# Optimization experiments

Hardware: AMD Instinct MI355X
Metric: run time of the kernel (lower is better)

Reference implementation:

```python
import jax, jax.numpy as jnp
import numpy as np

EMBED = 256; DEPTH = 64; DEPTH_START = 1.0
POS_RANGE = (-61.2, -61.2, -10.0, 61.2, 61.2, 10.0)
PC_RANGE = (-51.2, -51.2, -5.0, 51.2, 51.2, 3.0)
MEM_LEN = 512; TOPK = 256; NUM_Q = 900; NUM_CLS = 10; CODE = 10; L = 6
B, N, H, W = 4, 6, 16, 44
PAD_H, PAD_W = 256, 704
TWO_PI = 2.0 * np.pi


def _posemb(coords, nf=128):
    # sine/cosine embedding per coordinate channel -> [..., C, nf]
    dim_t = 10000.0 ** (2.0 * (jnp.arange(nf, dtype=jnp.float32) // 2) / nf)
    p = (coords * TWO_PI)[..., None] / dim_t
    p = jnp.stack([jnp.sin(p[..., 0::2]), jnp.cos(p[..., 1::2])], -1)
    return p.reshape(p.shape[:-2] + (nf,))


def _mlp2(x, W1, b1, W2, b2):
    return jnp.maximum(x @ W1 + b1, 0.0) @ W2 + b2


def _conv1x1(x, Wt, b):
    return jnp.einsum('bchw,co->bohw', x, Wt) + b[None, :, None, None]


def _ln(x, g, b):
    m = jnp.mean(x, -1, keepdims=True)
    v = jnp.mean(jnp.square(x - m), -1, keepdims=True)
    return (x - m) / jnp.sqrt(v + 1e-5) * g + b


def _sine_pe(not_mask):
    # SinePositionalEncoding2D, normalize=True; not_mask: [BN,H,W] float
    nf = EMBED // 2; eps = 1e-6
    y = jnp.cumsum(not_mask, 1); x = jnp.cumsum(not_mask, 2)
    y = y / (y[:, -1:, :] + eps) * TWO_PI
    x = x / (x[:, :, -1:] + eps) * TWO_PI
    dim_t = 10000.0 ** (2.0 * (jnp.arange(nf, dtype=jnp.float32) // 2) / nf)
    px = x[..., None] / dim_t; py = y[..., None] / dim_t
    px = jnp.stack([jnp.sin(px[..., 0::2]), jnp.cos(px[..., 1::2])], -1).reshape(x.shape + (nf,))
    py = jnp.stack([jnp.sin(py[..., 0::2]), jnp.cos(py[..., 1::2])], -1).reshape(y.shape + (nf,))
    return jnp.concatenate([py, px], -1).transpose(0, 3, 1, 2)  # [BN,EMBED,H,W]


def _forward(feat, lidar2img, prev_exists, memory_embedding, memory_reference_point,
             memory_timestamp, outs_dec, ref_pts, ip_w, ip_b, pe_w1, pe_b1, pe_w2, pe_b2,
             ap_w1, ap_b1, ap_w2, ap_b2, qe_w1, qe_b1, qe_w2, qe_b2, te_w1, te_b1, te_w2,
             te_b2, cls_w1, cls_b1, cls_g1, cls_be1, cls_w2, cls_b2, cls_g2, cls_be2,
             cls_w3, cls_b3, reg_w1, reg_b1, reg_w2, reg_b2, reg_w3, reg_b3, masks):
    b, n, c, h, w = feat.shape
    # --- pre_update_memory: memory_refresh + timestamp advance ---
    prev = prev_exists.reshape(b, 1, 1)
    mem_e = memory_embedding * prev
    mem_r = memory_reference_point * prev
    mem_t = memory_timestamp * prev + prev
    # --- input projection (1x1 conv) ---
    x = _conv1x1(feat.reshape(b * n, c, h, w), ip_w, ip_b).reshape(b, n, EMBED, h, w)
    # --- 3D position embedding (PETR frustum) ---
    coords_h = jnp.arange(h, dtype=jnp.float32) * (float(PAD_H) / h)
    coords_w = jnp.arange(w, dtype=jnp.float32) * (float(PAD_W) / w)
    d = jnp.arange(DEPTH, dtype=jnp.float32)
    bin_size = (POS_RANGE[3] - DEPTH_START) / (DEPTH * (1.0 + DEPTH))
    coords_d = DEPTH_START + bin_size * d * (d + 1.0)  # LID discretization
    cw, ch_, cd = jnp.meshgrid(coords_w, coords_h, coords_d, indexing='ij')  # [W,H,D]
    xy = jnp.stack([cw, ch_], -1) * jnp.maximum(cd, 1e-5)[..., None]
    coords4 = jnp.concatenate([xy, cd[..., None], jnp.ones_like(cd[..., None])], -1)  # [W,H,D,4]
    img2lidars = jnp.linalg.inv(lidar2img)  # [B,N,4,4]
    c3 = jnp.einsum('bnij,whdj->bnwhdi', img2lidars, coords4)[..., :3]  # [B,N,W,H,D,3]
    lo = jnp.asarray(POS_RANGE[:3], jnp.float32); hi = jnp.asarray(POS_RANGE[3:], jnp.float32)
    c3 = (c3 - lo) / (hi - lo)
    cmask = ((c3 > 1.0) | (c3 < 0.0)).reshape(b, n, w, h, DEPTH * 3).sum(-1) > DEPTH * 0.5
    coords_mask = masks | cmask.transpose(0, 1, 3, 2)
    c3 = c3.transpose(0, 1, 4, 5, 3, 2).reshape(b * n, DEPTH * 3, h, w)
    c3 = jnp.clip(c3, 0.0, 1.0)
    c3 = jnp.log(jnp.clip(c3, 1e-5, None) / jnp.clip(1.0 - c3, 1e-5, None))  # inverse_sigmoid
    coords_pos = _conv1x1(jnp.maximum(_conv1x1(c3, pe_w1, pe_b1), 0.0), pe_w2, pe_b2)
    coords_pos = coords_pos.reshape(b, n, EMBED, h, w)
    # --- 2D sine PE + adapt_pos3d ---
    sine = _sine_pe((~masks).astype(jnp.float32).reshape(b * n, h, w))
    sine = _conv1x1(jnp.maximum(_conv1x1(sine, ap_w1, ap_b1), 0.0), ap_w2, ap_b2)
    pos_embed = coords_pos + sine.reshape(b, n, EMBED, h, w)
    # --- query / time embeddings ---
    qp = _posemb(ref_pts)  # [Q,3,128]
    qp = jnp.concatenate([qp[:, 1], qp[:, 0], qp[:, 2]], -1)  # (y,x,z) -> [Q,384]
    query_pos = _mlp2(qp, qe_w1, qe_b1, qe_w2, qe_b2)  # [Q,256]
    tp = _posemb(mem_t)[..., 0, :]  # [B,M,128]
    time_emb = _mlp2(tp, te_w1, te_b1, te_w2, te_b2)  # [B,M,256]
    # --- cls / reg branches, stacked over decoder layers ---
    hc = jnp.maximum(_ln(jnp.einsum('lbqd,lde->lbqe', outs_dec, cls_w1) + cls_b1[:, None, None], cls_g1[:, None, None], cls_be1[:, None, None]), 0.0)
    hc = jnp.maximum(_ln(jnp.einsum('lbqd,lde->lbqe', hc, cls_w2) + cls_b2[:, None, None], cls_g2[:, None, None], cls_be2[:, None, None]), 0.0)
    all_cls = jnp.einsum('lbqd,ldc->lbqc', hc, cls_w3) + cls_b3[:, None, None]
    hr = jnp.maximum(jnp.einsum('lbqd,lde->lbqe', outs_dec, reg_w1) + reg_b1[:, None, None], 0.0)
    hr = jnp.maximum(jnp.einsum('lbqd,lde->lbqe', hr, reg_w2) + reg_b2[:, None, None], 0.0)
    all_reg = jnp.einsum('lbqd,ldc->lbqc', hr, reg_w3) + reg_b3[:, None, None]
    # --- post_update_memory: sigmoid + topk + gather + rolling concat ---
    rec_score = jnp.max(jax.nn.sigmoid(all_cls[-1]), -1)  # topk(1) over classes == max
    _, idx = jax.lax.top_k(rec_score, TOPK)  # [B,K]
    rec_mem = jax.lax.stop_gradient(jnp.take_along_axis(outs_dec[-1], idx[..., None], axis=1))
    rec_ref = jax.lax.stop_gradient(jnp.take_along_axis(all_reg[-1][..., :3], idx[..., None], axis=1))
    pmin = jnp.asarray(PC_RANGE[:3], jnp.float32); pmax = jnp.asarray(PC_RANGE[3:], jnp.float32)
    rec_ref = jnp.clip((rec_ref - pmin) / jnp.clip(pmax - pmin, 1e-5, None), 0.0, 1.0)
    rec_ts = jnp.zeros((b, TOPK, 1), rec_mem.dtype)
    new_mem_e = jnp.concatenate([rec_mem, mem_e], 1)[:, :MEM_LEN]
    new_mem_r = jnp.concatenate([rec_ref, mem_r], 1)[:, :MEM_LEN]
    new_mem_t = jnp.concatenate([rec_ts, mem_t], 1)[:, :MEM_LEN]
    return (all_cls, all_reg, new_mem_e, new_mem_r, new_mem_t, pos_embed, x, query_pos, time_emb, coords_mask)


def setup_inputs() -> dict:
    key = jax.random.key(0)
    ks = jax.random.split(key, 24)
    def rn(k, shape, s=0.02):
        return jax.random.normal(k, shape, jnp.float32) * s
    inp = dict(
        feat=jax.random.normal(ks[0], (B, N, 256, H, W), jnp.float32),
        lidar2img=jnp.eye(4, dtype=jnp.float32) + 0.05 * jax.random.normal(ks[1], (B, N, 4, 4), jnp.float32),
        prev_exists=jnp.array([1.0, 0.0, 1.0, 1.0], jnp.float32),
        memory_embedding=jax.random.normal(ks[2], (B, MEM_LEN, EMBED), jnp.float32),
        memory_reference_point=jax.random.uniform(ks[3], (B, MEM_LEN, 3)),
        memory_timestamp=jax.random.uniform(ks[4], (B, MEM_LEN, 1)),
        outs_dec=jax.random.normal(ks[5], (L, B, NUM_Q, EMBED), jnp.float32),
        ref_pts=jax.random.uniform(ks[6], (NUM_Q, 3)),
        ip_w=rn(ks[7], (256, EMBED)), ip_b=jnp.zeros(EMBED),
        pe_w1=rn(ks[8], (3 * DEPTH, EMBED * 2)), pe_b1=jnp.zeros(EMBED * 2),
        pe_w2=rn(ks[9], (EMBED * 2, EMBED)), pe_b2=jnp.zeros(EMBED),
        ap_w1=rn(ks[10], (EMBED, EMBED)), ap_b1=jnp.zeros(EMBED),
        ap_w2=rn(ks[11], (EMBED, EMBED)), ap_b2=jnp.zeros(EMBED),
        qe_w1=rn(ks[12], (EMBED * 3 // 2, EMBED)), qe_b1=jnp.zeros(EMBED),
        qe_w2=rn(ks[13], (EMBED, EMBED)), qe_b2=jnp.zeros(EMBED),
        te_w1=rn(ks[14], (EMBED // 2, EMBED)), te_b1=jnp.zeros(EMBED),
        te_w2=rn(ks[15], (EMBED, EMBED)), te_b2=jnp.zeros(EMBED),
        cls_w1=rn(ks[16], (L, EMBED, EMBED)), cls_b1=jnp.zeros((L, EMBED)),
        cls_g1=jnp.ones((L, EMBED)), cls_be1=jnp.zeros((L, EMBED)),
        cls_w2=rn(ks[17], (L, EMBED, EMBED)), cls_b2=jnp.zeros((L, EMBED)),
        cls_g2=jnp.ones((L, EMBED)), cls_be2=jnp.zeros((L, EMBED)),
        cls_w3=rn(ks[18], (L, EMBED, NUM_CLS)), cls_b3=jnp.zeros((L, NUM_CLS)),
        reg_w1=rn(ks[19], (L, EMBED, EMBED)), reg_b1=jnp.zeros((L, EMBED)),
        reg_w2=rn(ks[20], (L, EMBED, EMBED)), reg_b2=jnp.zeros((L, EMBED)),
        reg_w3=rn(ks[21], (L, EMBED, CODE)), reg_b3=jnp.zeros((L, CODE)),
        masks=jnp.zeros((B, N, H, W), bool),
    )
    return inp


def reference(feat, lidar2img, prev_exists, memory_embedding, memory_reference_point,
              memory_timestamp, outs_dec, ref_pts, ip_w, ip_b, pe_w1, pe_b1, pe_w2, pe_b2,
              ap_w1, ap_b1, ap_w2, ap_b2, qe_w1, qe_b1, qe_w2, qe_b2, te_w1, te_b1, te_w2,
              te_b2, cls_w1, cls_b1, cls_g1, cls_be1, cls_w2, cls_b2, cls_g2, cls_be2,
              cls_w3, cls_b3, reg_w1, reg_b1, reg_w2, reg_b2, reg_w3, reg_b3, masks):
    return _forward(feat, lidar2img, prev_exists, memory_embedding, memory_reference_point,
                    memory_timestamp, outs_dec, ref_pts, ip_w, ip_b, pe_w1, pe_b1, pe_w2, pe_b2,
                    ap_w1, ap_b1, ap_w2, ap_b2, qe_w1, qe_b1, qe_w2, qe_b2, te_w1, te_b1, te_w2,
                    te_b2, cls_w1, cls_b1, cls_g1, cls_be1, cls_w2, cls_b2, cls_g2, cls_be2,
                    cls_w3, cls_b3, reg_w1, reg_b1, reg_w2, reg_b2, reg_w3, reg_b3, masks)
```

## Files before the change

### kernel.cpp

```cpp
#include <hip/hip_runtime.h>
#include <math.h>


typedef unsigned short u16;
typedef __attribute__((ext_vector_type(8))) short short8v;
typedef __attribute__((ext_vector_type(4))) float f32x4;

#define DI __device__ __forceinline__
DI u16 f2bf(float f) {
    unsigned x = __float_as_uint(f);
    return (u16)((x + 0x7fffu + ((x >> 16) & 1u)) >> 16);
}
DI float bf2f(u16 u) { return __uint_as_float(((unsigned)u) << 16); }

#define TWO_PI_F 6.283185307179586f

__global__ void k_inv(const float* __restrict__ l2i, float* __restrict__ out) {
    int t = threadIdx.x;
    if (t >= 24) return;
    float a[4][8];
    for (int i = 0; i < 4; i++)
        for (int j = 0; j < 4; j++) {
            a[i][j] = l2i[t * 16 + i * 4 + j];
            a[i][4 + j] = (i == j) ? 1.f : 0.f;
        }
    for (int c = 0; c < 4; c++) {
        int p = c; float mv = fabsf(a[c][c]);
        for (int r = c + 1; r < 4; r++) {
            float v = fabsf(a[r][c]);
            if (v > mv) { mv = v; p = r; }
        }
        if (p != c)
            for (int j = 0; j < 8; j++) { float tmp = a[c][j]; a[c][j] = a[p][j]; a[p][j] = tmp; }
        float ip = 1.f / a[c][c];
        for (int j = 0; j < 8; j++) a[c][j] *= ip;
        for (int r = 0; r < 4; r++) {
            if (r == c) continue;
            float f = a[r][c];
            for (int j = 0; j < 8; j++) a[r][j] -= f * a[c][j];
        }
    }
    for (int i = 0; i < 4; i++)
        for (int j = 0; j < 4; j++)
            out[t * 16 + i * 4 + j] = a[i][4 + j];
}

__global__ __launch_bounds__(256) void k_memtail(
    const float* __restrict__ me, const float* __restrict__ mr, const float* __restrict__ mt,
    const float* __restrict__ prev,
    float* __restrict__ oe, float* __restrict__ orr, float* __restrict__ ot) {
    int b = blockIdx.x >> 8, j = blockIdx.x & 255, o = threadIdx.x;
    float pv = prev[b];
    oe[(size_t)(b * 512 + 256 + j) * 256 + o] = me[(size_t)(b * 512 + j) * 256 + o] * pv;
    if (o < 3)
        orr[(size_t)(b * 512 + 256 + j) * 3 + o] = mr[(size_t)(b * 512 + j) * 3 + o] * pv;
    if (o == 0) {
        ot[b * 512 + 256 + j] = mt[b * 512 + j] * pv + pv;
        ot[b * 512 + j] = 0.f;
    }
}

__global__ __launch_bounds__(256) void k_frustum(
    const float* __restrict__ inv, u16* __restrict__ c3aT, float* __restrict__ cm) {
    int pix = blockIdx.x * 4 + (threadIdx.x >> 6);
    int d = threadIdx.x & 63;
    int bn = pix / 704, p = pix - bn * 704;
    int h = p / 44, w = p - h * 44;
    const float* M = inv + bn * 16;
    float cw = w * 16.0f, ch = h * 16.0f;
    const float bin = (61.2f - 1.0f) / (64.0f * 65.0f);
    float cd = 1.0f + (bin * d) * (d + 1.0f);
    float xx = cw * cd, yy = ch * cd;
    float px = M[0] * xx + M[1] * yy + M[2] * cd + M[3];
    float py = M[4] * xx + M[5] * yy + M[6] * cd + M[7];
    float pz = M[8] * xx + M[9] * yy + M[10] * cd + M[11];
    float c[3];
    c[0] = (px + 61.2f) * (1.f / 122.4f);
    c[1] = (py + 61.2f) * (1.f / 122.4f);
    c[2] = (pz + 10.0f) * (1.f / 20.0f);
    u16* o = c3aT + (size_t)pix * 192 + d * 3;
    int cnt = 0;
#pragma unroll
    for (int i = 0; i < 3; i++) {
        cnt += ((c[i] > 1.0f) || (c[i] < 0.0f)) ? 1 : 0;
        float cc = fminf(fmaxf(c[i], 0.f), 1.f);
        float num = fmaxf(cc, 1e-5f);
        float den = fmaxf(1.0f - cc, 1e-5f);
        o[i] = f2bf(logf(num / den));
    }
    for (int off = 32; off; off >>= 1) cnt += __shfl_down(cnt, off);
    if (d == 0) cm[pix] = (cnt > 32) ? 1.f : 0.f;
}

__global__ __launch_bounds__(256) void k_sinebase(float* __restrict__ out) {
    int idx = blockIdx.x * 256 + threadIdx.x;
    if (idx >= 256 * 704) return;
    int c = idx / 704, p = idx - c * 704;
    int h = p / 44, w = p - h * 44;
    float pos = (c < 128) ? (h + 1) * (TWO_PI_F / (16.0f + 1e-6f))
                          : (w + 1) * (TWO_PI_F / (44.0f + 1e-6f));
    int cc = c & 127, k = cc >> 1;
    float dt = powf(10000.f, k * (1.f / 64.f));
    float arg = pos / dt;
    out[idx] = (cc & 1) ? cosf(arg) : sinf(arg);
}

template <int MODE>
DI void mlp_body(int blk, const float* __restrict__ src, const float* __restrict__ prev,
                 const float* __restrict__ w1, const float* __restrict__ b1,
                 const float* __restrict__ w2, const float* __restrict__ b2,
                 float* __restrict__ out,
                 float (*Ws)[32][256], float (*fin)[384], float (*h1)[256]) {
    constexpr int KF = MODE ? 384 : 128;
    constexpr int T1 = KF / 32;
    constexpr int TT = T1 + 8;
    const int tid = threadIdx.x;
    const int r0 = blk * 4;
    const int r = tid >> 6;
    const int c4 = (tid & 63) << 2;
    const int srow = tid >> 6;
    const int scol = (tid & 63) << 2;

    for (int i = tid; i < 4 * KF; i += 256) {
        int rr = i / KF, f = i - rr * KF;
        int row = r0 + rr;
        float arg;
        int fl;
        if (MODE == 0) {
            float pv = prev[row >> 9];
            float mt = src[row] * pv + pv;
            float dt = powf(10000.f, (f >> 1) * (1.f / 64.f));
            arg = mt * TWO_PI_F / dt;
            fl = f;
        } else {
            int seg = f >> 7, ff = f & 127;
            int cidx = (seg == 0) ? 1 : ((seg == 1) ? 0 : 2);
            float rv = src[row * 3 + cidx];
            float dt = powf(10000.f, (ff >> 1) * (1.f / 64.f));
            arg = rv * TWO_PI_F / dt;
            fl = ff;
        }
        fin[rr][f] = (fl & 1) ? cosf(arg) : sinf(arg);
    }

    float4 tmp4[8];
    auto stage_load = [&](int t) {
        const float* W = (t < T1) ? w1 + (size_t)t * 32 * 256
                                  : w2 + (size_t)(t - T1) * 32 * 256;
#pragma unroll
        for (int j = 0; j < 8; j++)
            tmp4[j] = *(const float4*)&W[(size_t)(j * 4 + srow) * 256 + scol];
    };
    auto stage_write = [&](int t) {
        const int bufi = t & 1;
#pragma unroll
        for (int j = 0; j < 8; j++)
            *(float4*)&Ws[bufi][j * 4 + srow][scol] = tmp4[j];
    };

    float acc1[4] = {}, acc2[4] = {};

    stage_load(0); stage_write(0);
    for (int t = 0; t < TT; t++) {
        __syncthreads();
        if (t + 1 < TT) stage_load(t + 1);
        const float* fr = (t < T1) ? &fin[r][t * 32] : &h1[r][(t - T1) * 32];
        if (t < T1) {
#pragma unroll
            for (int k = 0; k < 32; k++) {
                float fv = fr[k];
                const float4 wv = *(const float4*)&Ws[t & 1][k][c4];
                acc1[0] += fv * wv.x; acc1[1] += fv * wv.y;
                acc1[2] += fv * wv.z; acc1[3] += fv * wv.w;
            }
            if (t == T1 - 1) {
                float4 bv = *(const float4*)&b1[c4];
                float4 h4;
                h4.x = fmaxf(acc1[0] + bv.x, 0.f);
                h4.y = fmaxf(acc1[1] + bv.y, 0.f);
                h4.z = fmaxf(acc1[2] + bv.z, 0.f);
                h4.w = fmaxf(acc1[3] + bv.w, 0.f);
                *(float4*)&h1[r][c4] = h4;
            }
        } else {
#pragma unroll
            for (int k = 0; k < 32; k++) {
                float fv = fr[k];
                const float4 wv = *(const float4*)&Ws[t & 1][k][c4];
                acc2[0] += fv * wv.x; acc2[1] += fv * wv.y;
                acc2[2] += fv * wv.z; acc2[3] += fv * wv.w;
            }
        }
        if (t + 1 < TT) stage_write(t + 1);
    }
    {
        float4 bv = *(const float4*)&b2[c4];
        float4 o4;
        o4.x = acc2[0] + bv.x; o4.y = acc2[1] + bv.y;
        o4.z = acc2[2] + bv.z; o4.w = acc2[3] + bv.w;
        *(float4*)&out[(size_t)(r0 + r) * 256 + c4] = o4;
    }
}

__global__ __launch_bounds__(256) void k_mlp2(
    const float* __restrict__ memt, const float* __restrict__ prev,
    const float* __restrict__ te_w1, const float* __restrict__ te_b1,
    const float* __restrict__ te_w2, const float* __restrict__ te_b2,
    float* __restrict__ o_te,
    const float* __restrict__ rp,
    const float* __restrict__ qe_w1, const float* __restrict__ qe_b1,
    const float* __restrict__ qe_w2, const float* __restrict__ qe_b2,
    float* __restrict__ o_qp) {
    __shared__ __align__(16) float Ws[2][32][256];
    __shared__ __align__(16) float fin[4][384];
    __shared__ __align__(16) float h1[4][256];
    int blk = blockIdx.x;
    if (blk < 512)
        mlp_body<0>(blk, memt, prev, te_w1, te_b1, te_w2, te_b2, o_te, Ws, fin, h1);
    else
        mlp_body<1>(blk - 512, rp, prev, qe_w1, qe_b1, qe_w2, qe_b2, o_qp, Ws, fin, h1);
}

__global__ __launch_bounds__(256) void k_wtr4(
    const float* __restrict__ s0, const float* __restrict__ s1,
    const float* __restrict__ s2, const float* __restrict__ s3,
    u16* __restrict__ d0, u16* __restrict__ d1, u16* __restrict__ d2, u16* __restrict__ d3,
    int K, int N, int zper) {
    __shared__ float sh[32][33];
    int z = blockIdx.z, ti = z / zper, zz = z - ti * zper;
    const float* src = (ti == 0 ? s0 : ti == 1 ? s1 : ti == 2 ? s2 : s3) + (size_t)zz * K * N;
    u16* dst = (ti == 0 ? d0 : ti == 1 ? d1 : ti == 2 ? d2 : d3) + (size_t)zz * K * N;
    int n0 = blockIdx.x * 32, k0 = blockIdx.y * 32;
    int tx = threadIdx.x & 31, ty = threadIdx.x >> 5;
#pragma unroll
    for (int r = 0; r < 4; r++)
        sh[ty + 8 * r][tx] = src[(size_t)(k0 + ty + 8 * r) * N + n0 + tx];
    __syncthreads();
#pragma unroll
    for (int r = 0; r < 4; r++)
        dst[(size_t)(n0 + ty + 8 * r) * K + k0 + tx] = f2bf(sh[tx][ty + 8 * r]);
}

template <int AF32, int BTRANS, int BF32, int OUTF32, int ADD, int BIASM>
__global__ __launch_bounds__(256) void k_mfma(
    const void* __restrict__ Av, const void* __restrict__ B1v, const void* __restrict__ B2v,
    const float* __restrict__ bias1, const float* __restrict__ bias2,
    const float* __restrict__ add, void* __restrict__ outv,
    int M, int N, int K, int lda, int ldb, int ldo,
    long aZ, long bZ, long biasZ, long oZ, int zsplit, int zrelu, int aFull) {
    __shared__ __align__(16) u16 As[64][40];
    __shared__ __align__(16) u16 Bs[128][40];
    const int tid = threadIdx.x;
    const int z = blockIdx.z;
    const int zz = (z < zsplit) ? z : z - zsplit;
    const void* Bv = (z < zsplit) ? B1v : B2v;
    const float* bias = ((z < zsplit) ? bias1 : bias2) + (size_t)zz * biasZ;
    const bool relu = (z >= zrelu);
    const long aOff = (long)(aFull ? z : zz) * aZ;
    const long bOff = (long)zz * bZ;
    const int m0 = blockIdx.y * 64, n0 = blockIdx.x * 128;
    const int wave = tid >> 6, lane = tid & 63, quad = lane >> 4, l16 = lane & 15;
    const int wm = (wave >> 1) * 32, wn = (wave & 1) * 64;
    const int ar = tid & 63, ak = (tid >> 6) << 3;
    const int br = tid & 127, bk = (tid >> 7) << 4;
    f32x4 acc[2][4] = {};

    float pAf[8]; uint4 pAu = make_uint4(0, 0, 0, 0);
    float pBf[16]; u16 pBh[16];
    uint4 pBu0 = make_uint4(0, 0, 0, 0), pBu1 = make_uint4(0, 0, 0, 0);

    auto loadA = [&](int kt) {
        int gm = m0 + ar;
        if (AF32) {
#pragma unroll
            for (int q = 0; q < 8; q++) pAf[q] = 0.f;
            if (gm < M) {
                const float* ap = (const float*)Av + aOff + (size_t)gm * lda + kt + ak;
                float4 f0 = *(const float4*)ap;
                float4 f1 = *(const float4*)(ap + 4);
                pAf[0] = f0.x; pAf[1] = f0.y; pAf[2] = f0.z; pAf[3] = f0.w;
                pAf[4] = f1.x; pAf[5] = f1.y; pAf[6] = f1.z; pAf[7] = f1.w;
            }
        } else {
            pAu = make_uint4(0, 0, 0, 0);
            if (gm < M)
                pAu = *(const uint4*)((const u16*)Av + aOff + (size_t)gm * lda + kt + ak);
        }
    };
    auto storeA = [&]() {
        if (AF32) {
            uint4 u;
            u.x = f2bf(pAf[0]) | ((unsigned)f2bf(pAf[1]) << 16);
            u.y = f2bf(pAf[2]) | ((unsigned)f2bf(pAf[3]) << 16);
            u.z = f2bf(pAf[4]) | ((unsigned)f2bf(pAf[5]) << 16);
            u.w = f2bf(pAf[6]) | ((unsigned)f2bf(pAf[7]) << 16);
            *(uint4*)&As[ar][ak] = u;
        } else {
            *(uint4*)&As[ar][ak] = pAu;
        }
    };
    auto loadB = [&](int kt) {
        int gn = n0 + br;
        if (!BTRANS) {
            pBu0 = make_uint4(0, 0, 0, 0);
            pBu1 = make_uint4(0, 0, 0, 0);
            if (gn < N) {
                const u16* bp = (const u16*)Bv + bOff + (size_t)gn * ldb + kt + bk;
                pBu0 = *(const uint4*)bp;
                pBu1 = *(const uint4*)(bp + 8);
            }
        } else if (BF32) {
#pragma unroll
            for (int kk = 0; kk < 16; kk++)
                pBf[kk] = (gn < N) ? ((const float*)Bv + bOff)[(size_t)(kt + bk + kk) * ldb + gn]
                                   : 0.f;
        } else {
#pragma unroll
            for (int kk = 0; kk < 16; kk++)
                pBh[kk] = (gn < N) ? ((const u16*)Bv + bOff)[(size_t)(kt + bk + kk) * ldb + gn]
                                   : (u16)0;
        }
    };
    auto storeB = [&]() {
        if (!BTRANS) {
            *(uint4*)&Bs[br][bk] = pBu0;
            *(uint4*)&Bs[br][bk + 8] = pBu1;
        } else {
            u16 t[16];
#pragma unroll
            for (int kk = 0; kk < 16; kk++) t[kk] = BF32 ? f2bf(pBf[kk]) : pBh[kk];
            uint4 u0, u1;
            u0.x = t[0] | ((unsigned)t[1] << 16);
            u0.y = t[2] | ((unsigned)t[3] << 16);
            u0.z = t[4] | ((unsigned)t[5] << 16);
            u0.w = t[6] | ((unsigned)t[7] << 16);
            u1.x = t[8] | ((unsigned)t[9] << 16);
            u1.y = t[10] | ((unsigned)t[11] << 16);
            u1.z = t[12] | ((unsigned)t[13] << 16);
            u1.w = t[14] | ((unsigned)t[15] << 16);
            *(uint4*)&Bs[br][bk] = u0;
            *(uint4*)&Bs[br][bk + 8] = u1;
        }
    };

    loadA(0); loadB(0);
    for (int kt = 0; kt < K; kt += 32) {
        storeA(); storeB();
        __syncthreads();
        if (kt + 32 < K) { loadA(kt + 32); loadB(kt + 32); }
        short8v af[2], bfr[4];
#pragma unroll
        for (int i = 0; i < 2; i++) af[i] = *(const short8v*)&As[wm + i * 16 + l16][quad * 8];
#pragma unroll
        for (int j = 0; j < 4; j++) bfr[j] = *(const short8v*)&Bs[wn + j * 16 + l16][quad * 8];
#pragma unroll
        for (int i = 0; i < 2; i++)
#pragma unroll
            for (int j = 0; j < 4; j++)
                acc[i][j] = __builtin_amdgcn_mfma_f32_16x16x32_bf16(af[i], bfr[j], acc[i][j], 0, 0, 0);
        __syncthreads();
    }

    float* outf = (float*)outv + (size_t)z * oZ;
    u16* outh = (u16*)outv + (size_t)z * oZ;
#pragma unroll
    for (int i = 0; i < 2; i++) {
#pragma unroll
        for (int r = 0; r < 4; r++) {
            int row = m0 + wm + i * 16 + quad * 4 + r;
            if (row >= M) continue;
#pragma unroll
            for (int j = 0; j < 4; j++) {
                int col = n0 + wn + j * 16 + l16;
                if (col >= N) continue;
                float v = acc[i][j][r] + (BIASM ? bias[row] : bias[col]);
                if (relu) v = fmaxf(v, 0.f);
                if (ADD) v += add[(size_t)row * ldo + col];
                if (OUTF32) outf[(size_t)row * ldo + col] = v;
                else        outh[(size_t)row * ldo + col] = f2bf(v);
            }
        }
    }
}

__global__ __launch_bounds__(256) void k_sgemm(
    const float* __restrict__ A, const float* __restrict__ Bm,
    const float* __restrict__ bias, float* __restrict__ out, int M) {
    __shared__ __align__(16) float As[16][68];
    __shared__ __align__(16) float Bs[16][68];
    const int tid = threadIdx.x;
    const int m0 = blockIdx.y * 64, n0 = blockIdx.x * 64;
    const int tm = tid >> 4, tn = tid & 15;
    const int kA = tid >> 4, mA = (tid << 2) & 63;
    const int mN = tid & 63, kq = tid >> 6;
    float acc[4][4] = {};
    for (int kt = 0; kt < 256; kt += 16) {
        int gm = m0 + mN;
        float4 u = {0.f, 0.f, 0.f, 0.f};
        if (gm < M) u = *(const float4*)(A + (size_t)gm * 256 + kt + (kq << 2));
        As[(kq << 2) + 0][mN] = u.x; As[(kq << 2) + 1][mN] = u.y;
        As[(kq << 2) + 2][mN] = u.z; As[(kq << 2) + 3][mN] = u.w;
        {
            float4 b = *(const float4*)(Bm + (size_t)(kt + kA) * 256 + n0 + mA);
            Bs[kA][mA + 0] = b.x; Bs[kA][mA + 1] = b.y;
            Bs[kA][mA + 2] = b.z; Bs[kA][mA + 3] = b.w;
        }
        __syncthreads();
#pragma unroll
        for (int k = 0; k < 16; k++) {
            const float4 av = *(const float4*)(&As[k][tm << 2]);
            const float4 bv = *(const float4*)(&Bs[k][tn << 2]);
            float ar[4] = {av.x, av.y, av.z, av.w};
            float br[4] = {bv.x, bv.y, bv.z, bv.w};
#pragma unroll
            for (int i = 0; i < 4; i++)
#pragma unroll
                for (int j = 0; j < 4; j++) acc[i][j] = fmaf(ar[i], br[j], acc[i][j]);
        }
        __syncthreads();
    }
#pragma unroll
    for (int i = 0; i < 4; i++) {
        int row = m0 + (tm << 2) + i;
        if (row >= M) continue;
        float4 o4;
        o4.x = acc[i][0] + bias[n0 + (tn << 2) + 0];
        o4.y = acc[i][1] + bias[n0 + (tn << 2) + 1];
        o4.z = acc[i][2] + bias[n0 + (tn << 2) + 2];
        o4.w = acc[i][3] + bias[n0 + (tn << 2) + 3];
        *(float4*)(out + (size_t)row * 256 + n0 + (tn << 2)) = o4;
    }
}

__global__ __launch_bounds__(256) void k_lnb(
    u16* __restrict__ buf, const float* __restrict__ g, const float* __restrict__ be) {
    int tid = threadIdx.x, wid = tid >> 6, lane = tid & 63;
    int row = blockIdx.x * 4 + wid;
    int l = row / 3600;
    size_t base = (size_t)row * 256 + lane;
    float v[4];
#pragma unroll
    for (int i = 0; i < 4; i++) v[i] = bf2f(buf[base + (i << 6)]);
    float s = v[0] + v[1] + v[2] + v[3];
    for (int off = 32; off; off >>= 1) s += __shfl_down(s, off);
    s = __shfl(s, 0);
    float mean = s * (1.f / 256.f);
    float d[4], q = 0.f;
#pragma unroll
    for (int i = 0; i < 4; i++) { d[i] = v[i] - mean; q += d[i] * d[i]; }
    for (int off = 32; off; off >>= 1) q += __shfl_down(q, off);
    q = __shfl(q, 0);
    float rstd = rsqrtf(q * (1.f / 256.f) + 1e-5f);
#pragma unroll
    for (int i = 0; i < 4; i++) {
        int c = lane + (i << 6);
        buf[base + (i << 6)] = f2bf(fmaxf(d[i] * rstd * g[l * 256 + c] + be[l * 256 + c], 0.f));
    }
}

__global__ __launch_bounds__(256) void k_ln5(
    float* __restrict__ buf, const float* __restrict__ g, const float* __restrict__ be) {
    int tid = threadIdx.x, wid = tid >> 6, lane = tid & 63;
    int row = blockIdx.x * 4 + wid;
    size_t base = (size_t)row * 256 + lane;
    float v[4];
#pragma unroll
    for (int i = 0; i < 4; i++) v[i] = buf[base + (i << 6)];
    float s = v[0] + v[1] + v[2] + v[3];
    for (int off = 32; off; off >>= 1) s += __shfl_down(s, off);
    s = __shfl(s, 0);
    float mean = s * (1.f / 256.f);
    float d[4], q = 0.f;
#pragma unroll
    for (int i = 0; i < 4; i++) { d[i] = v[i] - mean; q += d[i] * d[i]; }
    for (int off = 32; off; off >>= 1) q += __shfl_down(q, off);
    q = __shfl(q, 0);
    float rstd = rsqrtf(q * (1.f / 256.f) + 1e-5f);
#pragma unroll
    for (int i = 0; i < 4; i++) {
        int c = lane + (i << 6);
        buf[base + (i << 6)] = fmaxf(d[i] * rstd * g[c] + be[c], 0.f);
    }
}

__global__ __launch_bounds__(320) void k_heads_cls(
    const u16* __restrict__ hc, const float* __restrict__ wc, const float* __restrict__ bc,
    float* __restrict__ ocls, int lbase) {
    __shared__ u16 sh[32][256];
    int z = blockIdx.z, l = lbase + z, tb = blockIdx.x * 32, tid = threadIdx.x;
    for (int i = tid; i < 8192; i += 320) {
        int rr = i >> 8, k = i & 255;
        int tok = tb + rr;
        sh[rr][k] = (tok < 3600) ? hc[(size_t)(z * 3600 + tok) * 256 + k] : (u16)0;
    }
    __syncthreads();
    int tl = tid / 10, o = tid - tl * 10;
    const float* w = wc + l * 2560 + o;
    float ac = 0.f;
    for (int k = 0; k < 256; k++) ac += bf2f(sh[tl][k]) * w[k * 10];
    ac += bc[l * 10 + o];
    int tok = tb + tl;
    if (tok < 3600) ocls[(size_t)(l * 3600 + tok) * 10 + o] = ac;
}

__global__ __launch_bounds__(320) void k_heads_reg(
    const u16* __restrict__ hr, const float* __restrict__ wr, const float* __restrict__ br,
    float* __restrict__ oreg, float* __restrict__ reg3, int lbase) {
    __shared__ u16 sh[32][256];
    int z = blockIdx.z, l = lbase + z, tb = blockIdx.x * 32, tid = threadIdx.x;
    for (int i = tid; i < 8192; i += 320) {
        int rr = i >> 8, k = i & 255;
        int tok = tb + rr;
        sh[rr][k] = (tok < 3600) ? hr[(size_t)(z * 3600 + tok) * 256 + k] : (u16)0;
    }
    __syncthreads();
    int tl = tid / 10, o = tid - tl * 10;
    const float* w = wr + l * 2560 + o;
    float ar = 0.f;
    for (int k = 0; k < 256; k++) ar += bf2f(sh[tl][k]) * w[k * 10];
    ar += br[l * 10 + o];
    int tok = tb + tl;
    if (tok < 3600) {
        oreg[(size_t)(l * 3600 + tok) * 10 + o] = ar;
        if (l == 5 && o < 3) reg3[tok * 3 + o] = ar;
    }
}

__global__ __launch_bounds__(320) void k_score(
    const float* __restrict__ h2, const float* __restrict__ wc, const float* __restrict__ bc,
    float* __restrict__ score) {
    __shared__ float sh[32][256];
    __shared__ float clsv[32][10];
    int tb = blockIdx.x * 32, tid = threadIdx.x;
    for (int i = tid; i < 8192; i += 320) {
        int rr = i >> 8, k = i & 255;
        int tok = tb + rr;
        sh[rr][k] = (tok < 3600) ? h2[(size_t)tok * 256 + k] : 0.f;
    }
    __syncthreads();
    int tl = tid / 10, o = tid - tl * 10;
    const float* w = wc + 5 * 2560 + o;
    float ac = 0.f;
    for (int k = 0; k < 256; k++) ac += sh[tl][k] * w[k * 10];
    ac += bc[5 * 10 + o];
    int tok = tb + tl;
    if (tok < 3600) clsv[tl][o] = ac;
    __syncthreads();
    if (tid < 32 && tb + tid < 3600) {
        float m = clsv[tid][0];
#pragma unroll
        for (int c = 1; c < 10; c++) m = fmaxf(m, clsv[tid][c]);
        score[tb + tid] = m;
    }
}

__global__ __launch_bounds__(1024) void k_sel(
    const float* __restrict__ score, int* __restrict__ sel) {
    __shared__ float sc[900];
    int b = blockIdx.x, tid = threadIdx.x;
    for (int i = tid; i < 900; i += 1024) sc[i] = score[b * 900 + i];
    __syncthreads();
    if (tid < 900) {
        float s = sc[tid];
        int r = 0;
        for (int j = 0; j < 900; j++) {
            float sj = sc[j];
            r += ((sj > s) || (sj == s && j < tid)) ? 1 : 0;
        }
        if (r < 256) sel[b * 256 + r] = tid;
    }
}

__global__ __launch_bounds__(256) void k_gather(
    const int* __restrict__ sel, const float* __restrict__ reg3,
    const float* __restrict__ od, float* __restrict__ oe, float* __restrict__ orr) {
    int b = blockIdx.y;
    int r = blockIdx.x * 4 + (threadIdx.x >> 6);
    int lane = threadIdx.x & 63;
    int q = sel[b * 256 + r];
    const float4* src = (const float4*)(od + (size_t)((20 + b) * 900 + q) * 256);
    float4* dst = (float4*)(oe + (size_t)(b * 512 + r) * 256);
    dst[lane] = src[lane];
    if (lane == 0) {
#pragma unroll
        for (int kk = 0; kk < 3; kk++) {
            float v = reg3[(b * 900 + q) * 3 + kk];
            float lo = (kk == 2) ? -5.0f : -51.2f;
            float rng = (kk == 2) ? 8.0f : 102.4f;
            orr[(size_t)(b * 512 + r) * 3 + kk] = fminf(fmaxf((v - lo) / rng, 0.f), 1.f);
        }
    }
}

extern "C" void kernel_launch(void* const* d_in, const int* in_sizes, int n_in,
                              void* d_out, int out_size, void* d_ws, size_t ws_size,
                              hipStream_t stream) {
    const float* feat   = (const float*)d_in[0];
    const float* l2i    = (const float*)d_in[1];
    const float* prev   = (const float*)d_in[2];
    const float* meme   = (const float*)d_in[3];
    const float* memr   = (const float*)d_in[4];
    const float* memt   = (const float*)d_in[5];
    const float* od     = (const float*)d_in[6];
    const float* rp     = (const float*)d_in[7];
    const float* ip_w   = (const float*)d_in[8];
    const float* ip_b   = (const float*)d_in[9];
    const float* pe_w1  = (const float*)d_in[10];
    const float* pe_b1  = (const float*)d_in[11];
    const float* pe_w2  = (const float*)d_in[12];
    const float* pe_b2  = (const float*)d_in[13];
    const float* ap_w1  = (const float*)d_in[14];
    const float* ap_b1  = (const float*)d_in[15];
    const float* ap_w2  = (const float*)d_in[16];
    const float* ap_b2  = (const float*)d_in[17];
    const float* qe_w1  = (const float*)d_in[18];
    const float* qe_b1  = (const float*)d_in[19];
    const float* qe_w2  = (const float*)d_in[20];
    const float* qe_b2  = (const float*)d_in[21];
    const float* te_w1  = (const float*)d_in[22];
    const float* te_b1  = (const float*)d_in[23];
    const float* te_w2  = (const float*)d_in[24];
    const float* te_b2  = (const float*)d_in[25];
    const float* cls_w1 = (const float*)d_in[26];
    const float* cls_b1 = (const float*)d_in[27];
    const float* cls_g1 = (const float*)d_in[28];
    const float* cls_be1= (const float*)d_in[29];
    const float* cls_w2 = (const float*)d_in[30];
    const float* cls_b2 = (const float*)d_in[31];
    const float* cls_g2 = (const float*)d_in[32];
    const float* cls_be2= (const float*)d_in[33];
    const float* cls_w3 = (const float*)d_in[34];
    const float* cls_b3 = (const float*)d_in[35];
    const float* reg_w1 = (const float*)d_in[36];
    const float* reg_b1 = (const float*)d_in[37];
    const float* reg_w2 = (const float*)d_in[38];
    const float* reg_b2 = (const float*)d_in[39];
    const float* reg_w3 = (const float*)d_in[40];
    const float* reg_b3 = (const float*)d_in[41];

    float* o32    = (float*)d_out;
    float* o_cls  = o32;
    float* o_reg  = o32 + 216000;
    float* o_meme = o32 + 432000;
    float* o_memr = o32 + 956288;
    float* o_memt = o32 + 962432;
    float* o_pos  = o32 + 964480;
    float* o_x    = o32 + 5289856;
    float* o_qp   = o32 + 9615232;
    float* o_te   = o32 + 9845632;
    float* o_cm   = o32 + 10369920;

    u16*   h1b  = (u16*)(o32 + 432000);
    u16*   h2b  = (u16*)(o32 + 3196800);
    u16*   w1Tc = (u16*)(o32 + 5961600);
    u16*   w1Tr = (u16*)(o32 + 6158208);
    u16*   w2Tc = (u16*)(o32 + 6354816);
    u16*   w2Tr = (u16*)(o32 + 6551424);
    float* h1f  = o32 + 432000;
    float* h2f  = o32 + 1353600;
    u16*   c3aT = (u16*)(o32 + 964480);
    float* sineb = o32 + 432000;
    float* sinea = o32 + 612224;
    u16*   hapb  = (u16*)(o32 + 792448);
    u16*   h1pe  = (u16*)(o32 + 5289856);
    u16*   pe1T  = (u16*)(o32 + 9615232);
    u16*   pe2T  = (u16*)(o32 + 9664384);
    u16*   ap1T  = (u16*)(o32 + 9729920);
    u16*   ap2T  = (u16*)(o32 + 9762688);
    float* w_score = o32 + 9845632;
    float* w_reg3  = o32 + 9849232;
    float* w_inv   = o32 + 9860032;
    int*   w_sel   = (int*)(o32 + 9860416);
    u16*   ipT     = (u16*)(o32 + 9861440);

    k_inv<<<1, 32, 0, stream>>>(l2i, w_inv);

    k_wtr4<<<dim3(8, 8, 24), 256, 0, stream>>>(cls_w1, reg_w1, cls_w2, reg_w2,
                                               w1Tc, w1Tr, w2Tc, w2Tr, 256, 256, 6);
    k_wtr4<<<dim3(16, 6, 1), 256, 0, stream>>>(pe_w1, pe_w1, pe_w1, pe_w1,
                                               pe1T, pe1T, pe1T, pe1T, 192, 512, 1);
    k_wtr4<<<dim3(8, 16, 1), 256, 0, stream>>>(pe_w2, pe_w2, pe_w2, pe_w2,
                                               pe2T, pe2T, pe2T, pe2T, 512, 256, 1);
    k_wtr4<<<dim3(8, 8, 3), 256, 0, stream>>>(ip_w, ap_w1, ap_w2, ap_w2,
                                              ipT, ap1T, ap2T, ap2T, 256, 256, 1);

    k_mfma<1, 0, 0, 0, 0, 0><<<dim3(2, 57, 6), 256, 0, stream>>>(
        od, w1Tc, w1Tc, cls_b1, cls_b1, nullptr, h1b,
        3600, 256, 256, 256, 256, 256, 921600, 65536, 256, 921600, 99, 99, 0);
    k_lnb<<<5400, 256, 0, stream>>>(h1b, cls_g1, cls_be1);
    k_mfma<0, 0, 0, 0, 0, 0><<<dim3(2, 57, 6), 256, 0, stream>>>(
        h1b, w2Tc, w2Tc, cls_b2, cls_b2, nullptr, h2b,
        3600, 256, 256, 256, 256, 256, 921600, 65536, 256, 921600, 99, 99, 1);
    k_lnb<<<5400, 256, 0, stream>>>(h2b, cls_g2, cls_be2);
    k_heads_cls<<<dim3(113, 1, 6), 320, 0, stream>>>(h2b, cls_w3, cls_b3, o_cls, 0);

    k_mfma<1, 0, 0, 0, 0, 0><<<dim3(2, 57, 6), 256, 0, stream>>>(
        od, w1Tr, w1Tr, reg_b1, reg_b1, nullptr, h1b,
        3600, 256, 256, 256, 256, 256, 921600, 65536, 256, 921600, 99, 0, 0);
    k_mfma<0, 0, 0, 0, 0, 0><<<dim3(2, 57, 6), 256, 0, stream>>>(
        h1b, w2Tr, w2Tr, reg_b2, reg_b2, nullptr, h2b,
        3600, 256, 256, 256, 256, 256, 921600, 65536, 256, 921600, 99, 0, 1);
    k_heads_reg<<<dim3(113, 1, 6), 320, 0, stream>>>(h2b, reg_w3, reg_b3, o_reg, w_reg3, 0);

    k_sgemm<<<dim3(4, 57), 256, 0, stream>>>(od + (size_t)5 * 921600, cls_w1 + 5 * 65536,
                                             cls_b1 + 5 * 256, h1f, 3600);
    k_ln5<<<900, 256, 0, stream>>>(h1f, cls_g1 + 5 * 256, cls_be1 + 5 * 256);
    k_sgemm<<<dim3(4, 57), 256, 0, stream>>>(h1f, cls_w2 + 5 * 65536, cls_b2 + 5 * 256, h2f, 3600);
    k_ln5<<<900, 256, 0, stream>>>(h2f, cls_g2 + 5 * 256, cls_be2 + 5 * 256);
    k_score<<<113, 320, 0, stream>>>(h2f, cls_w3, cls_b3, w_score);

    k_frustum<<<4224, 256, 0, stream>>>(w_inv, c3aT, o_cm);
    k_sinebase<<<704, 256, 0, stream>>>(sineb);
    k_mfma<0, 1, 1, 0, 0, 1><<<dim3(6, 4, 1), 256, 0, stream>>>(
        ap1T, sineb, sineb, ap_b1, ap_b1, nullptr, hapb,
        256, 704, 256, 256, 704, 704, 0, 0, 0, 0, 99, 0, 0);
    k_mfma<0, 1, 0, 1, 0, 1><<<dim3(6, 4, 1), 256, 0, stream>>>(
        ap2T, hapb, hapb, ap_b2, ap_b2, nullptr, sinea,
        256, 704, 256, 256, 704, 704, 0, 0, 0, 0, 99, 99, 0);
    k_mfma<0, 0, 0, 0, 0, 1><<<dim3(6, 8, 24), 256, 0, stream>>>(
        pe1T, c3aT, c3aT, pe_b1, pe_b1, nullptr, h1pe,
        512, 704, 192, 192, 192, 704, 0, 135168, 0, 360448, 99, 0, 0);
    k_mfma<0, 1, 0, 1, 1, 1><<<dim3(6, 4, 24), 256, 0, stream>>>(
        pe2T, h1pe, h1pe, pe_b2, pe_b2, sinea, o_pos,
        256, 704, 512, 512, 704, 704, 0, 360448, 0, 180224, 99, 99, 0);
    k_mfma<0, 1, 1, 1, 0, 1><<<dim3(6, 4, 24), 256, 0, stream>>>(
        ipT, feat, feat, ip_b, ip_b, nullptr, o_x,
        256, 704, 256, 256, 704, 704, 0, 180224, 0, 180224, 99, 99, 0);

    k_memtail<<<1024, 256, 0, stream>>>(meme, memr, memt, prev, o_meme, o_memr, o_memt);
    k_sel<<<4, 1024, 0, stream>>>(w_score, w_sel);
    k_gather<<<dim3(64, 4), 256, 0, stream>>>(w_sel, w_reg3, od, o_meme, o_memr);

    k_mlp2<<<737, 256, 0, stream>>>(memt, prev, te_w1, te_b1, te_w2, te_b2, o_te,
                                    rp, qe_w1, qe_b1, qe_w2, qe_b2, o_qp);
}
```

Before: 594.5 us.

## Process 16 rows per block in MLP kernel with 4x4 register tiles

The fused positional-embedding MLP kernel now handles 16 rows per block instead of 4. Each thread computes a 4x4 output tile from transposed feature and hidden buffers in shared memory, so every weight tile staged from global memory is reused across four times as many rows. The block count drops from 737 to 185, and the register double-buffered weight prefetch is replaced by a simpler single-buffer load-then-sync loop. This cuts redundant weight traffic, at the cost of less parallelism, no overlap of loads with compute, and clamped or guarded padding rows for the 900-query tail.

```diff
diff --git a/kernel.cpp b/kernel.cpp
--- a/kernel.cpp
+++ b/kernel.cpp
@@ -110,95 +110,105 @@
                  const float* __restrict__ w1, const float* __restrict__ b1,
                  const float* __restrict__ w2, const float* __restrict__ b2,
                  float* __restrict__ out,
-                 float (*Ws)[32][256], float (*fin)[384], float (*h1)[256]) {
+                 float (*finT)[16], float (*h1T)[20], float (*Ws)[256]) {
     constexpr int KF = MODE ? 384 : 128;
     constexpr int T1 = KF / 32;
-    constexpr int TT = T1 + 8;
+    constexpr int MROWS = MODE ? 900 : 2048;
     const int tid = threadIdx.x;
-    const int r0 = blk * 4;
-    const int r = tid >> 6;
-    const int c4 = (tid & 63) << 2;
-    const int srow = tid >> 6;
-    const int scol = (tid & 63) << 2;
-
-    for (int i = tid; i < 4 * KF; i += 256) {
-        int rr = i / KF, f = i - rr * KF;
-        int row = r0 + rr;
+    const int r0 = blk * 16;
+    const int w4 = (tid >> 6) * 4;
+    const int c4 = (tid & 63) * 4;
+
+    for (int i = tid; i < 16 * KF; i += 256) {
+        int r = i & 15, f = i >> 4;
+        int row = r0 + r;
+        int rs = (row < MROWS) ? row : (MROWS - 1);
         float arg;
         int fl;
         if (MODE == 0) {
-            float pv = prev[row >> 9];
-            float mt = src[row] * pv + pv;
+            float pv = prev[rs >> 9];
+            float mt = src[rs] * pv + pv;
             float dt = powf(10000.f, (f >> 1) * (1.f / 64.f));
             arg = mt * TWO_PI_F / dt;
             fl = f;
         } else {
             int seg = f >> 7, ff = f & 127;
             int cidx = (seg == 0) ? 1 : ((seg == 1) ? 0 : 2);
-            float rv = src[row * 3 + cidx];
+            float rv = src[rs * 3 + cidx];
             float dt = powf(10000.f, (ff >> 1) * (1.f / 64.f));
             arg = rv * TWO_PI_F / dt;
             fl = ff;
         }
-        fin[rr][f] = (fl & 1) ? cosf(arg) : sinf(arg);
-    }
-
-    float4 tmp4[8];
-    auto stage_load = [&](int t) {
-        const float* W = (t < T1) ? w1 + (size_t)t * 32 * 256
-                                  : w2 + (size_t)(t - T1) * 32 * 256;
-#pragma unroll
-        for (int j = 0; j < 8; j++)
-            tmp4[j] = *(const float4*)&W[(size_t)(j * 4 + srow) * 256 + scol];
+        finT[f][r] = (fl & 1) ? cosf(arg) : sinf(arg);
+    }
+
+    auto stage = [&](const float* __restrict__ W, int t) {
+        const float4* W4 = (const float4*)(W + (size_t)t * 32 * 256);
+        float4* S4 = (float4*)Ws;
+        float4 tmp[8];
+#pragma unroll
+        for (int j = 0; j < 8; j++) tmp[j] = W4[tid + j * 256];
+#pragma unroll
+        for (int j = 0; j < 8; j++) S4[tid + j * 256] = tmp[j];
     };
-    auto stage_write = [&](int t) {
-        const int bufi = t & 1;
-#pragma unroll
-        for (int j = 0; j < 8; j++)
-            *(float4*)&Ws[bufi][j * 4 + srow][scol] = tmp4[j];
-    };
-
-    float acc1[4] = {}, acc2[4] = {};
-
-    stage_load(0); stage_write(0);
-    for (int t = 0; t < TT; t++) {
+
+    float acc1[4][4] = {};
+    for (int t = 0; t < T1; t++) {
+        stage(w1, t);
         __syncthreads();
-        if (t + 1 < TT) stage_load(t + 1);
-        const float* fr = (t < T1) ? &fin[r][t * 32] : &h1[r][(t - T1) * 32];
-        if (t < T1) {
-#pragma unroll
-            for (int k = 0; k < 32; k++) {
-                float fv = fr[k];
-                const float4 wv = *(const float4*)&Ws[t & 1][k][c4];
-                acc1[0] += fv * wv.x; acc1[1] += fv * wv.y;
-                acc1[2] += fv * wv.z; acc1[3] += fv * wv.w;
-            }
-            if (t == T1 - 1) {
-                float4 bv = *(const float4*)&b1[c4];
-                float4 h4;
-                h4.x = fmaxf(acc1[0] + bv.x, 0.f);
-                h4.y = fmaxf(acc1[1] + bv.y, 0.f);
-                h4.z = fmaxf(acc1[2] + bv.z, 0.f);
-                h4.w = fmaxf(acc1[3] + bv.w, 0.f);
-                *(float4*)&h1[r][c4] = h4;
-            }
-        } else {
-#pragma unroll
-            for (int k = 0; k < 32; k++) {
-                float fv = fr[k];
-                const float4 wv = *(const float4*)&Ws[t & 1][k][c4];
-                acc2[0] += fv * wv.x; acc2[1] += fv * wv.y;
-                acc2[2] += fv * wv.z; acc2[3] += fv * wv.w;
-            }
-        }
-        if (t + 1 < TT) stage_write(t + 1);
+#pragma unroll 4
+        for (int k = 0; k < 32; k++) {
+            float4 fv = *(const float4*)&finT[t * 32 + k][w4];
+            float4 wv = *(const float4*)&Ws[k][c4];
+            float fa[4] = {fv.x, fv.y, fv.z, fv.w};
+            float wa[4] = {wv.x, wv.y, wv.z, wv.w};
+#pragma unroll
+            for (int i = 0; i < 4; i++)
+#pragma unroll
+                for (int j = 0; j < 4; j++) acc1[i][j] = fmaf(fa[i], wa[j], acc1[i][j]);
+        }
+        __syncthreads();
+    }
+    {
+        float4 bv = *(const float4*)&b1[c4];
+        float ba[4] = {bv.x, bv.y, bv.z, bv.w};
+#pragma unroll
+        for (int i = 0; i < 4; i++)
+#pragma unroll
+            for (int j = 0; j < 4; j++)
+                h1T[c4 + j][w4 + i] = fmaxf(acc1[i][j] + ba[j], 0.f);
+    }
+
+    float acc2[4][4] = {};
+    for (int t = 0; t < 8; t++) {
+        stage(w2, t);
+        __syncthreads();
+#pragma unroll 4
+        for (int k = 0; k < 32; k++) {
+            float4 fv = *(const float4*)&h1T[t * 32 + k][w4];
+            float4 wv = *(const float4*)&Ws[k][c4];
+            float fa[4] = {fv.x, fv.y, fv.z, fv.w};
+            float wa[4] = {wv.x, wv.y, wv.z, wv.w};
+#pragma unroll
+            for (int i = 0; i < 4; i++)
+#pragma unroll
+                for (int j = 0; j < 4; j++) acc2[i][j] = fmaf(fa[i], wa[j], acc2[i][j]);
+        }
+        __syncthreads();
     }
     {
         float4 bv = *(const float4*)&b2[c4];
-        float4 o4;
-        o4.x = acc2[0] + bv.x; o4.y = acc2[1] + bv.y;
-        o4.z = acc2[2] + bv.z; o4.w = acc2[3] + bv.w;
-        *(float4*)&out[(size_t)(r0 + r) * 256 + c4] = o4;
+#pragma unroll
+        for (int i = 0; i < 4; i++) {
+            int row = r0 + w4 + i;
+            if (row >= MROWS) continue;
+            float4 o4;
+            o4.x = acc2[i][0] + bv.x;
+            o4.y = acc2[i][1] + bv.y;
+            o4.z = acc2[i][2] + bv.z;
+            o4.w = acc2[i][3] + bv.w;
+            *(float4*)&out[(size_t)row * 256 + c4] = o4;
+        }
     }
 }
 
@@ -211,14 +221,14 @@
     const float* __restrict__ qe_w1, const float* __restrict__ qe_b1,
     const float* __restrict__ qe_w2, const float* __restrict__ qe_b2,
     float* __restrict__ o_qp) {
-    __shared__ __align__(16) float Ws[2][32][256];
-    __shared__ __align__(16) float fin[4][384];
-    __shared__ __align__(16) float h1[4][256];
+    __shared__ __align__(16) float finT[384][16];
+    __shared__ __align__(16) float h1T[256][20];
+    __shared__ __align__(16) float Ws[32][256];
     int blk = blockIdx.x;
-    if (blk < 512)
-        mlp_body<0>(blk, memt, prev, te_w1, te_b1, te_w2, te_b2, o_te, Ws, fin, h1);
+    if (blk < 128)
+        mlp_body<0>(blk, memt, prev, te_w1, te_b1, te_w2, te_b2, o_te, finT, h1T, Ws);
     else
-        mlp_body<1>(blk - 512, rp, prev, qe_w1, qe_b1, qe_w2, qe_b2, o_qp, Ws, fin, h1);
+        mlp_body<1>(blk - 128, rp, prev, qe_w1, qe_b1, qe_w2, qe_b2, o_qp, finT, h1T, Ws);
 }
 
 __global__ __launch_bounds__(256) void k_wtr4(
@@ -731,6 +741,6 @@
     k_sel<<<4, 1024, 0, stream>>>(w_score, w_sel);
     k_gather<<<dim3(64, 4), 256, 0, stream>>>(w_sel, w_reg3, od, o_meme, o_memr);
 
-    k_mlp2<<<737, 256, 0, stream>>>(memt, prev, te_w1, te_b1, te_w2, te_b2, o_te,
+    k_mlp2<<<185, 256, 0, stream>>>(memt, prev, te_w1, te_b1, te_w2, te_b2, o_te,
                                     rp, qe_w1, qe_b1, qe_w2, qe_b2, o_qp);
 }
```

Result: no change. 593.7 us (-0.1%).
